# Kernel tuning notes

Measured on AMD Instinct MI355X. Metric: run time of the kernel, lower is better.

Reference implementation:

```python
import jax, jax.numpy as jnp
import numpy as np

EPS = 1e-08

def setup_inputs() -> dict:
    key = jax.random.key(0)
    k1, k2, k3, k4 = jax.random.split(key, 4)
    B, T, D, D_sample = 16, 512, 2048, 4096
    z_hist = jax.random.normal(k1, (B, T, D), dtype=jnp.float32)
    decay_rates = jax.random.normal(k2, (D_sample,), dtype=jnp.float32)
    idx_i = jax.random.randint(k3, (D_sample,), 0, D)
    idx_j = jax.random.randint(k4, (D_sample,), 0, D)
    return {"z_hist": z_hist, "decay_rates": decay_rates, "idx_i": idx_i, "idx_j": idx_j}

def reference(z_hist, decay_rates, idx_i, idx_j):
    B, T, D = z_hist.shape
    r = jax.nn.softplus(decay_rates)                      # [N]
    times = jnp.arange(T, dtype=z_hist.dtype)             # [T]
    # decay[t, n] = exp(-r_n * (T - 1 - t))
    decay = jnp.exp(-r[None, :] * (T - 1 - times)[:, None])  # [T, N]
    z_i = z_hist[:, :, idx_i]                              # [B, T, N]
    z_j = z_hist[:, :, idx_j]                              # [B, T, N]
    num = jnp.einsum('btn,btn,tn->bn', z_i, z_j, decay)    # [B, N]
    den = jnp.sqrt(decay.sum(axis=0) + EPS)                # [N]
    return num / den[None, :]
```

## Files before the change

kernel.cpp:

```cpp
#include <hip/hip_runtime.h>
#include <math.h>

#define B_    16
#define T_    512
#define D_    2048
#define DS_   4096
#define TG_   128
#define RS_   2052
#define EPS_  1e-8f
#define CLOG  16.0f


__device__ __forceinline__ float softplus_f(float x) {
    return (x > 20.f) ? x : log1pf(expf(x));
}

__device__ __forceinline__ void glds16(const float* g, float* l) {
    __builtin_amdgcn_global_load_lds((const __attribute__((address_space(1))) void*)g,
                                     (__attribute__((address_space(3))) void*)l,
                                     16, 0, 0);
}

__global__ __launch_bounds__(1024) void prep_kernel(const float* __restrict__ decay_rates,
                                                    float* __restrict__ inv_den,
                                                    float* __restrict__ g_u,
                                                    float* __restrict__ nr_u,
                                                    int* __restrict__ nout_s,
                                                    int* __restrict__ tgmin_g,
                                                    int* __restrict__ smax_g) {
    __shared__ int hist[64];
    __shared__ int start_s[64];
    __shared__ int tgl[16];
    const int tid = threadIdx.x;
    if (tid < 64) hist[tid] = 0;
    __syncthreads();
    float rv[4]; int qv[4];
    #pragma unroll
    for (int k = 0; k < 4; ++k) {
        int n = tid + k * 1024;
        float r = softplus_f(decay_rates[n]);
        rv[k] = r;
        float hf = CLOG / r;
        int h = (hf >= 511.f) ? 511 : (int)hf;
        qv[k] = h >> 3;
        atomicAdd(&hist[qv[k]], 1);
        float S = expm1f(-r * (float)T_) / expm1f(-r);
        inv_den[n] = 1.0f / sqrtf(S + EPS_);
        g_u[n]     = expf(r);
        nr_u[n]    = -r;
    }
    __syncthreads();
    if (tid == 0) {
        int run = 0;
        for (int q = 63; q >= 0; --q) { start_s[q] = run; run += hist[q]; }
    }
    __syncthreads();
    if (tid < 64) hist[tid] = start_s[tid];
    if (tid >= 64 && tid < 80) {
        int s = tid - 64;
        int R = s * 256;
        int qs = 0;
        for (int q = 63; q >= 0; --q) {
            int nxt = (q == 0) ? DS_ : start_s[q - 1];
            if (start_s[q] <= R && R < nxt) { qs = q; break; }
        }
        int h = (qs << 3) | 7;
        int tm = (511 - h) >> 2; if (tm < 0) tm = 0;
        tgl[s] = tm;
        tgmin_g[s] = tm;
    }
    __syncthreads();
    if (tid < TG_) {
        int c = 0;
        #pragma unroll
        for (int s = 0; s < 16; ++s) c += (tgl[s] <= tid) ? 1 : 0;
        smax_g[tid] = c;
    }
    #pragma unroll
    for (int k = 0; k < 4; ++k) {
        int n = tid + k * 1024;
        int pos = atomicAdd(&hist[qv[k]], 1);
        nout_s[pos] = n;
    }
}

__global__ __launch_bounds__(256) void main_kernel(const float* __restrict__ z,
                                                   const float* __restrict__ g_u,
                                                   const float* __restrict__ nr_u,
                                                   const int* __restrict__ idx_i,
                                                   const int* __restrict__ idx_j,
                                                   const int* __restrict__ nout_s,
                                                   const int* __restrict__ smax_g,
                                                   float* __restrict__ num) {
    __shared__ float rows[4 * RS_];
    const int tg   = blockIdx.x;
    const int b    = blockIdx.y;
    const int tid  = threadIdx.x;
    const int wave = tid >> 6, lane = tid & 63;
    const int tb   = tg * 4;

    const float* src = z + ((size_t)b * T_ + tb + wave) * D_ + lane * 4;
    float* dst = rows + wave * RS_;
    #pragma unroll
    for (int s = 0; s < 8; ++s)
        glds16(src + s * 256, dst + s * 256);

    const int smax = smax_g[tg];
    const float kb0 = (float)(511 - tb);
    int pair[16]; float g[16], w0[16];
    #pragma unroll
    for (int s = 0; s < 16; ++s) {
        if (s < smax) {
            int m = tid + s * 256;
            int n = nout_s[m];
            pair[s] = idx_i[n] | (idx_j[n] << 16);
            g[s]    = g_u[n];
            w0[s]   = __expf(nr_u[n] * kb0);
        }
    }

    asm volatile("s_waitcnt vmcnt(0)" ::: "memory");
    __syncthreads();

    #pragma unroll
    for (int s = 0; s < 16; ++s) {
        if (s < smax) {
            int ci = pair[s] & 0xFFFF, cj = pair[s] >> 16;
            float vi0 = rows[ci],           vj0 = rows[cj];
            float vi1 = rows[RS_ + ci],     vj1 = rows[RS_ + cj];
            float vi2 = rows[2 * RS_ + ci], vj2 = rows[2 * RS_ + cj];
            float vi3 = rows[3 * RS_ + ci], vj3 = rows[3 * RS_ + cj];
            float gs = g[s];
            float h3 = vi3 * vj3;
            float h2 = fmaf(h3, gs, vi2 * vj2);
            float h1 = fmaf(h2, gs, vi1 * vj1);
            float h0 = fmaf(h1, gs, vi0 * vj0);
            num[((size_t)tg * B_ + b) * DS_ + tid + s * 256] = w0[s] * h0;
        }
    }
}

__global__ __launch_bounds__(256) void fin_kernel(const float* __restrict__ num,
                                                  const float* __restrict__ inv_den,
                                                  const int* __restrict__ nout_s,
                                                  const int* __restrict__ tgmin_g,
                                                  float* __restrict__ out) {
    int gt = blockIdx.x * 256 + threadIdx.x;
    int m  = gt & (DS_ - 1);
    int b  = gt >> 12;
    int tgmin = tgmin_g[m >> 8];
    float sum = 0.f;
    #pragma unroll 4
    for (int tg = tgmin; tg < TG_; ++tg)
        sum += num[((size_t)tg * B_ + b) * DS_ + m];
    int n = nout_s[m];
    out[b * DS_ + n] = sum * inv_den[n];
}

extern "C" void kernel_launch(void* const* d_in, const int* in_sizes, int n_in,
                              void* d_out, int out_size, void* d_ws, size_t ws_size,
                              hipStream_t stream) {
    const float* z  = (const float*)d_in[0];
    const float* dr = (const float*)d_in[1];
    const int*   ii = (const int*)d_in[2];
    const int*   jj = (const int*)d_in[3];
    float* out = (float*)d_out;

    float* num     = (float*)d_ws;
    float* inv_den = num + (size_t)TG_ * B_ * DS_;
    float* g_u     = inv_den + DS_;
    float* nr_u    = g_u + DS_;
    int*   nout_s  = (int*)(nr_u + DS_);
    int*   tgmin_g = nout_s + DS_;
    int*   smax_g  = tgmin_g + 16;

    hipLaunchKernelGGL(prep_kernel, dim3(1), dim3(1024), 0, stream,
                       dr, inv_den, g_u, nr_u, nout_s, tgmin_g, smax_g);
    hipLaunchKernelGGL(main_kernel, dim3(TG_, B_), dim3(256), 0, stream,
                       z, g_u, nr_u, ii, jj, nout_s, smax_g, num);
    hipLaunchKernelGGL(fin_kernel, dim3((B_ * DS_) / 256), dim3(256), 0, stream,
                       num, inv_den, nout_s, tgmin_g, out);
}
```

Before: 135.2 us.

## Replace partial-sum buffer and finalize kernel with atomic accumulation into output

Instead of writing per-time-group partial sums to a workspace and reducing them in a separate finalize kernel, the main kernel now folds the inverse denominator into the weight and atomically adds directly into the output, which is zeroed with a memset first. This removes the large intermediate buffer write/read and one kernel launch. In exchange it adds many float atomics to global memory, with contention from up to 128 time groups per output element, and the summation order becomes nondeterministic.

```diff
diff --git a/kernel.cpp b/kernel.cpp
--- a/kernel.cpp
+++ b/kernel.cpp
@@ -26,7 +26,6 @@
                                                     float* __restrict__ g_u,
                                                     float* __restrict__ nr_u,
                                                     int* __restrict__ nout_s,
-                                                    int* __restrict__ tgmin_g,
                                                     int* __restrict__ smax_g) {
     __shared__ int hist[64];
     __shared__ int start_s[64];
@@ -34,12 +33,11 @@
     const int tid = threadIdx.x;
     if (tid < 64) hist[tid] = 0;
     __syncthreads();
-    float rv[4]; int qv[4];
+    int qv[4];
     #pragma unroll
     for (int k = 0; k < 4; ++k) {
         int n = tid + k * 1024;
         float r = softplus_f(decay_rates[n]);
-        rv[k] = r;
         float hf = CLOG / r;
         int h = (hf >= 511.f) ? 511 : (int)hf;
         qv[k] = h >> 3;
@@ -67,7 +65,6 @@
         int h = (qs << 3) | 7;
         int tm = (511 - h) >> 2; if (tm < 0) tm = 0;
         tgl[s] = tm;
-        tgmin_g[s] = tm;
     }
     __syncthreads();
     if (tid < TG_) {
@@ -87,11 +84,12 @@
 __global__ __launch_bounds__(256) void main_kernel(const float* __restrict__ z,
                                                    const float* __restrict__ g_u,
                                                    const float* __restrict__ nr_u,
+                                                   const float* __restrict__ inv_den,
                                                    const int* __restrict__ idx_i,
                                                    const int* __restrict__ idx_j,
                                                    const int* __restrict__ nout_s,
                                                    const int* __restrict__ smax_g,
-                                                   float* __restrict__ num) {
+                                                   float* __restrict__ out) {
     __shared__ float rows[4 * RS_];
     const int tg   = blockIdx.x;
     const int b    = blockIdx.y;
@@ -107,15 +105,16 @@
 
     const int smax = smax_g[tg];
     const float kb0 = (float)(511 - tb);
-    int pair[16]; float g[16], w0[16];
+    int pair[16], nidx[16]; float g[16], w0[16];
     #pragma unroll
     for (int s = 0; s < 16; ++s) {
         if (s < smax) {
             int m = tid + s * 256;
             int n = nout_s[m];
+            nidx[s] = n;
             pair[s] = idx_i[n] | (idx_j[n] << 16);
             g[s]    = g_u[n];
-            w0[s]   = __expf(nr_u[n] * kb0);
+            w0[s]   = __expf(nr_u[n] * kb0) * inv_den[n];
         }
     }
 
@@ -135,26 +134,9 @@
             float h2 = fmaf(h3, gs, vi2 * vj2);
             float h1 = fmaf(h2, gs, vi1 * vj1);
             float h0 = fmaf(h1, gs, vi0 * vj0);
-            num[((size_t)tg * B_ + b) * DS_ + tid + s * 256] = w0[s] * h0;
+            atomicAdd(&out[b * DS_ + nidx[s]], w0[s] * h0);
         }
     }
-}
-
-__global__ __launch_bounds__(256) void fin_kernel(const float* __restrict__ num,
-                                                  const float* __restrict__ inv_den,
-                                                  const int* __restrict__ nout_s,
-                                                  const int* __restrict__ tgmin_g,
-                                                  float* __restrict__ out) {
-    int gt = blockIdx.x * 256 + threadIdx.x;
-    int m  = gt & (DS_ - 1);
-    int b  = gt >> 12;
-    int tgmin = tgmin_g[m >> 8];
-    float sum = 0.f;
-    #pragma unroll 4
-    for (int tg = tgmin; tg < TG_; ++tg)
-        sum += num[((size_t)tg * B_ + b) * DS_ + m];
-    int n = nout_s[m];
-    out[b * DS_ + n] = sum * inv_den[n];
 }
 
 extern "C" void kernel_launch(void* const* d_in, const int* in_sizes, int n_in,
@@ -166,18 +148,15 @@
     const int*   jj = (const int*)d_in[3];
     float* out = (float*)d_out;
 
-    float* num     = (float*)d_ws;
-    float* inv_den = num + (size_t)TG_ * B_ * DS_;
+    float* inv_den = (float*)d_ws;
     float* g_u     = inv_den + DS_;
     float* nr_u    = g_u + DS_;
     int*   nout_s  = (int*)(nr_u + DS_);
-    int*   tgmin_g = nout_s + DS_;
-    int*   smax_g  = tgmin_g + 16;
+    int*   smax_g  = nout_s + DS_;
 
+    hipMemsetAsync(d_out, 0, (size_t)out_size * sizeof(float), stream);
     hipLaunchKernelGGL(prep_kernel, dim3(1), dim3(1024), 0, stream,
-                       dr, inv_den, g_u, nr_u, nout_s, tgmin_g, smax_g);
+                       dr, inv_den, g_u, nr_u, nout_s, smax_g);
     hipLaunchKernelGGL(main_kernel, dim3(TG_, B_), dim3(256), 0, stream,
-                       z, g_u, nr_u, ii, jj, nout_s, smax_g, num);
-    hipLaunchKernelGGL(fin_kernel, dim3((B_ * DS_) / 256), dim3(256), 0, stream,
-                       num, inv_den, nout_s, tgmin_g, out);
+                       z, g_u, nr_u, inv_den, ii, jj, nout_s, smax_g, out);
 }
```

New measurement: 159.7 us. 1.18x slower.
